# Optimization experiments

Hardware: AMD Instinct MI355X
Metric: run time of the kernel (lower is better)

Reference implementation:

```python
import jax, jax.numpy as jnp
import numpy as np

EPS_LN = 1e-5

def layer_norm(x, g, b):
    mu = x.mean(-1, keepdims=True)
    var = ((x - mu) ** 2).mean(-1, keepdims=True)
    return (x - mu) / jnp.sqrt(var + EPS_LN) * g + b

def spike(x):
    # MultiSpike: quantized spike activation, forward = clip(round(x), 0, 4)
    return jnp.clip(jnp.round(x), 0.0, 4.0)

def setup_inputs() -> dict:
    key = jax.random.key(0)
    ks = jax.random.split(key, 8)
    B, C, H, W = 16, 256, 56, 56
    hid = 128
    inp = {}
    inp['feature_map'] = jax.random.normal(ks[0], (B, C, H, W), jnp.float32)
    inp['audio_feature'] = jax.random.normal(ks[1], (B, 1, C), jnp.float32)
    # MINE params
    inp['w1'] = jax.random.normal(ks[2], (hid, 2 * C), jnp.float32) / np.sqrt(2 * C)
    inp['b1'] = jnp.zeros((hid,), jnp.float32)
    inp['g1'] = jnp.ones((hid,), jnp.float32)
    inp['beta1'] = jnp.zeros((hid,), jnp.float32)
    inp['w2'] = jax.random.normal(ks[3], (hid // 2, hid), jnp.float32) / np.sqrt(hid)
    inp['b2'] = jnp.zeros((hid // 2,), jnp.float32)
    inp['g2'] = jnp.ones((hid // 2,), jnp.float32)
    inp['beta2'] = jnp.zeros((hid // 2,), jnp.float32)
    inp['w3'] = jax.random.normal(ks[4], (1, hid // 2), jnp.float32) / np.sqrt(hid // 2)
    inp['b3'] = jnp.zeros((1,), jnp.float32)
    # MI params
    inp['pw'] = jax.random.normal(ks[5], (C, C), jnp.float32) / np.sqrt(C)
    inp['pb'] = jnp.zeros((C,), jnp.float32)
    inp['pg'] = jnp.ones((C,), jnp.float32)
    inp['pbeta'] = jnp.zeros((C,), jnp.float32)
    return inp

def reference(feature_map, audio_feature, w1, b1, g1, beta1, w2, b2, g2, beta2,
              w3, b3, pw, pb, pg, pbeta):
    B, C, H, W = feature_map.shape
    # visual tokens: [B*H*W, C]
    visual = feature_map.transpose(0, 2, 3, 1).reshape(B * H * W, C)
    # broadcast audio to every spatial position: [B*H*W, C]
    audio = jnp.broadcast_to(audio_feature[:, 0][:, None, None, :], (B, H, W, C)).reshape(B * H * W, C)
    # MINE MLP on joint features
    joint = jnp.concatenate([visual, audio], axis=1)            # [BHW, 2C]
    h = spike(layer_norm(joint @ w1.T + b1, g1, beta1))          # [BHW, 128]
    h = spike(layer_norm(h @ w2.T + b2, g2, beta2))              # [BHW, 64]
    mi = (h @ w3.T + b3)[:, 0]                                   # [BHW]
    mi_map = mi.reshape(B, 1, H * W)
    fm_flat = feature_map.reshape(B, C, H * W)
    # MI-weighted pooling: [B,1,C]
    x = jnp.einsum('bos,bcs->boc', mi_map, fm_flat)
    x = x @ pw.T + pb                                            # proj (dropout = eval identity)
    x = spike(layer_norm(x, pg, pbeta))                          # [B,1,C]
    fusion_map = jnp.einsum('bchw,bc->bchw', feature_map, x[:, 0])
    mi4 = mi_map.reshape(B, 1, H, W)
    mi4 = (mi4 - mi4.min()) / (mi4.max() - mi4.min() + 1e-6)     # global min-max norm
    return fusion_map, mi4
```

## Files before the change

### kernel.cpp

```cpp
#include <hip/hip_runtime.h>

#define HW 3136
#define NPOS 12845056

__device__ __forceinline__ unsigned fkey(float f) {
  unsigned u = __float_as_uint(f);
  return (u & 0x80000000u) ? ~u : (u | 0x80000000u);
}
__device__ __forceinline__ float funkey(unsigned u) {
  return __uint_as_float((u & 0x80000000u) ? (u & 0x7FFFFFFFu) : ~u);
}
__device__ __forceinline__ float spikef(float x) {
  return fminf(fmaxf(rintf(x), 0.0f), 4.0f);
}

__global__ __launch_bounds__(256) void prep_kernel(
    const float* __restrict__ audio, const float* __restrict__ w1,
    const float* __restrict__ b1, const float* __restrict__ w2,
    float* __restrict__ a_pre, float* __restrict__ w1t,
    float* __restrict__ w2t, float* __restrict__ pool,
    unsigned* __restrict__ mm)
{
  __shared__ float au[256];
  const int bx = blockIdx.x, t = threadIdx.x;
  if (bx < 128) {
    int idx = bx * 256 + t;
    int c = idx >> 7, j = idx & 127;
    w1t[idx] = w1[j * 512 + c];
  } else if (bx < 160) {
    int idx = (bx - 128) * 256 + t;
    int k = idx >> 6, j2 = idx & 63;
    w2t[idx] = w2[j2 * 128 + k];
  } else if (bx < 176) {
    int b = bx - 160;
    au[t] = audio[b * 256 + t];
    __syncthreads();
    int w = t >> 6, l = t & 63;
    float a0 = au[l], a1 = au[l + 64], a2 = au[l + 128], a3 = au[l + 192];
    for (int jj = 0; jj < 32; ++jj) {
      int j = w * 32 + jj;
      const float* row = w1 + j * 512 + 256;
      float s = row[l] * a0 + row[l + 64] * a1 + row[l + 128] * a2 + row[l + 192] * a3;
      #pragma unroll
      for (int off = 32; off; off >>= 1) s += __shfl_xor(s, off);
      if (l == 0) a_pre[b * 128 + j] = s + b1[j];
    }
  } else {
    for (int i = t; i < 4096; i += 256) pool[i] = 0.0f;
    if (t == 0) { mm[0] = 0xFFFFFFFFu; mm[1] = 0u; }
  }
}

__global__ __launch_bounds__(256, 3) void mlp_kernel(
    const float* __restrict__ fm, const float* __restrict__ w1t,
    const float* __restrict__ w2t, const float* __restrict__ b2,
    const float* __restrict__ w3, const float* __restrict__ b3,
    const float* __restrict__ g1, const float* __restrict__ be1,
    const float* __restrict__ g2, const float* __restrict__ be2,
    const float* __restrict__ a_pre, float* __restrict__ mi_out,
    float* __restrict__ pool, unsigned* __restrict__ mm)
{
  __shared__ float h1f[128 * 64];
  __shared__ float red[8][64];

  const int b  = blockIdx.y;
  const int s0 = blockIdx.x * 64;
  const int t  = threadIdx.x;
  const int l  = t & 63;
  const int wv = __builtin_amdgcn_readfirstlane(t >> 6);

  const float* fmblk = fm + (size_t)b * 256 * HW + s0;

  float acc[32];
  #pragma unroll
  for (int j = 0; j < 32; ++j) acc[j] = 0.f;
  {
    const float*  fp = fmblk + l;
    const float4* wr = (const float4*)(w1t + wv * 32);
    #pragma unroll 4
    for (int k = 0; k < 256; ++k) {
      float x = *fp; fp += HW;
      #pragma unroll
      for (int q = 0; q < 8; ++q) {
        float4 w4 = wr[q];
        acc[4*q+0] = fmaf(x, w4.x, acc[4*q+0]);
        acc[4*q+1] = fmaf(x, w4.y, acc[4*q+1]);
        acc[4*q+2] = fmaf(x, w4.z, acc[4*q+2]);
        acc[4*q+3] = fmaf(x, w4.w, acc[4*q+3]);
      }
      wr += 32;
    }
  }
  {
    const float4* ap = (const float4*)(a_pre + b * 128 + wv * 32);
    #pragma unroll
    for (int q = 0; q < 8; ++q) {
      float4 a4 = ap[q];
      acc[4*q+0] += a4.x; acc[4*q+1] += a4.y;
      acc[4*q+2] += a4.z; acc[4*q+3] += a4.w;
    }
  }

  float mu, inv;
  {
    float s = 0.f;
    #pragma unroll
    for (int j = 0; j < 32; ++j) s += acc[j];
    red[wv][l] = s;
    __syncthreads();
    mu = (red[0][l] + red[1][l] + red[2][l] + red[3][l]) * (1.0f/128.0f);
    float s2 = 0.f;
    #pragma unroll
    for (int j = 0; j < 32; ++j) { float d = acc[j] - mu; s2 = fmaf(d, d, s2); }
    red[4 + wv][l] = s2;
    __syncthreads();
    float var = (red[4][l] + red[5][l] + red[6][l] + red[7][l]) * (1.0f/128.0f);
    inv = 1.0f / sqrtf(var + 1e-5f);
  }

  {
    const float* gp = g1  + wv * 32;
    const float* bp = be1 + wv * 32;
    #pragma unroll
    for (int j = 0; j < 32; ++j) {
      float h = spikef((acc[j] - mu) * inv * gp[j] + bp[j]);
      h1f[(wv * 32 + j) * 64 + l] = h;
    }
  }
  __syncthreads();

  float a2[16];
  #pragma unroll
  for (int j = 0; j < 16; ++j) a2[j] = 0.f;
  {
    const float*  hp = h1f + l;
    const float4* wr = (const float4*)(w2t + wv * 16);
    #pragma unroll 4
    for (int k = 0; k < 128; ++k) {
      float h = *hp; hp += 64;
      #pragma unroll
      for (int q = 0; q < 4; ++q) {
        float4 w4 = wr[q];
        a2[4*q+0] = fmaf(h, w4.x, a2[4*q+0]);
        a2[4*q+1] = fmaf(h, w4.y, a2[4*q+1]);
        a2[4*q+2] = fmaf(h, w4.z, a2[4*q+2]);
        a2[4*q+3] = fmaf(h, w4.w, a2[4*q+3]);
      }
      wr += 16;
    }
  }
  {
    const float4* bp = (const float4*)(b2 + wv * 16);
    #pragma unroll
    for (int q = 0; q < 4; ++q) {
      float4 b4 = bp[q];
      a2[4*q+0] += b4.x; a2[4*q+1] += b4.y;
      a2[4*q+2] += b4.z; a2[4*q+3] += b4.w;
    }
  }

  float mu2, inv2;
  {
    float s = 0.f;
    #pragma unroll
    for (int j = 0; j < 16; ++j) s += a2[j];
    red[wv][l] = s;
    __syncthreads();
    mu2 = (red[0][l] + red[1][l] + red[2][l] + red[3][l]) * (1.0f/64.0f);
    float s2 = 0.f;
    #pragma unroll
    for (int j = 0; j < 16; ++j) { float d = a2[j] - mu2; s2 = fmaf(d, d, s2); }
    red[4 + wv][l] = s2;
    __syncthreads();
    float var = (red[4][l] + red[5][l] + red[6][l] + red[7][l]) * (1.0f/64.0f);
    inv2 = 1.0f / sqrtf(var + 1e-5f);
  }

  {
    const float* gp = g2  + wv * 16;
    const float* bp = be2 + wv * 16;
    const float* wp = w3  + wv * 16;
    float p = 0.f;
    #pragma unroll
    for (int j = 0; j < 16; ++j) {
      float sp = spikef((a2[j] - mu2) * inv2 * gp[j] + bp[j]);
      p = fmaf(sp, wp[j], p);
    }
    red[wv][l] = p;
  }
  __syncthreads();
  const float mi = red[0][l] + red[1][l] + red[2][l] + red[3][l] + b3[0];

  if (wv == 0) {
    mi_out[b * HW + s0 + l] = mi;
    float mn = mi, mx = mi;
    #pragma unroll
    for (int off = 32; off; off >>= 1) {
      mn = fminf(mn, __shfl_xor(mn, off));
      mx = fmaxf(mx, __shfl_xor(mx, off));
    }
    if (l == 0) {
      unsigned kmn = fkey(mn), kmx = fkey(mx);
      volatile unsigned* vmm = (volatile unsigned*)mm;
      if (kmn < vmm[0]) atomicMin(&mm[0], kmn);
      if (kmx > vmm[1]) atomicMax(&mm[1], kmx);
    }
  }

  {
    const float* fp = fmblk + l + (size_t)(wv << 6) * HW;
    #pragma unroll 4
    for (int ci = 0; ci < 64; ++ci) {
      float v = *fp * mi; fp += HW;
      #pragma unroll
      for (int off = 32; off; off >>= 1) v += __shfl_xor(v, off);
      if (l == 0) atomicAdd(&pool[b * 256 + (wv << 6) + ci], v);
    }
  }
}

__global__ __launch_bounds__(256) void scale_kernel(
    const float* __restrict__ pool, const float* __restrict__ pw,
    const float* __restrict__ pb, const float* __restrict__ pg,
    const float* __restrict__ pbeta, float* __restrict__ scale,
    const unsigned* __restrict__ mm, float* __restrict__ gpar)
{
  __shared__ float pl[256];
  __shared__ float xsh[256];
  __shared__ float rs[4], rs2[4];
  int b = blockIdx.x, t = threadIdx.x;
  pl[t] = pool[b*256 + t];
  __syncthreads();
  int w = t >> 6, l = t & 63;
  float p0 = pl[l], p1 = pl[l+64], p2 = pl[l+128], p3 = pl[l+192];
  for (int jj = 0; jj < 64; ++jj) {
    int j = w*64 + jj;
    const float* row = pw + j*256;
    float s = row[l]*p0 + row[l+64]*p1 + row[l+128]*p2 + row[l+192]*p3;
    #pragma unroll
    for (int off = 32; off; off >>= 1) s += __shfl_xor(s, off);
    if (l == 0) xsh[j] = s;
  }
  __syncthreads();
  float x = xsh[t] + pb[t];
  float s = x;
  #pragma unroll
  for (int off = 32; off; off >>= 1) s += __shfl_xor(s, off);
  if (l == 0) rs[w] = s;
  __syncthreads();
  float mu = (rs[0]+rs[1]+rs[2]+rs[3]) * (1.0f/256.0f);
  float d = x - mu;
  float s2 = d*d;
  #pragma unroll
  for (int off = 32; off; off >>= 1) s2 += __shfl_xor(s2, off);
  if (l == 0) rs2[w] = s2;
  __syncthreads();
  float var = (rs2[0]+rs2[1]+rs2[2]+rs2[3]) * (1.0f/256.0f);
  float v = d / sqrtf(var + 1e-5f) * pg[t] + pbeta[t];
  scale[b*256 + t] = spikef(v);
  if (b == 0 && t == 0) {
    float mn = funkey(mm[0]), mx = funkey(mm[1]);
    gpar[0] = mn;
    gpar[1] = mx - mn + 1e-6f;
  }
}

__global__ __launch_bounds__(256) void fuse_kernel(
    const float4* __restrict__ fm4, const float* __restrict__ scale,
    const float4* __restrict__ mi4, const float* __restrict__ gpar,
    float4* __restrict__ out4, float4* __restrict__ mi4out)
{
  const int c = blockIdx.x, b = blockIdx.y, t = threadIdx.x;
  if (c < 256) {
    float s = scale[b * 256 + c];
    size_t base = ((size_t)b * 256 + c) * 784;
    #pragma unroll
    for (int i = 0; i < 3; ++i) {
      int idx = t + i * 256;
      float4 v = fm4[base + idx];
      out4[base + idx] = make_float4(v.x*s, v.y*s, v.z*s, v.w*s);
    }
    int idx = t + 768;
    if (idx < 784) {
      float4 v = fm4[base + idx];
      out4[base + idx] = make_float4(v.x*s, v.y*s, v.z*s, v.w*s);
    }
  } else {
    float gmin = gpar[0], den = gpar[1];
    size_t base = (size_t)b * 784;
    #pragma unroll
    for (int i = 0; i < 3; ++i) {
      int idx = t + i * 256;
      float4 v = mi4[base + idx];
      mi4out[base + idx] = make_float4((v.x-gmin)/den, (v.y-gmin)/den,
                                       (v.z-gmin)/den, (v.w-gmin)/den);
    }
    int idx = t + 768;
    if (idx < 784) {
      float4 v = mi4[base + idx];
      mi4out[base + idx] = make_float4((v.x-gmin)/den, (v.y-gmin)/den,
                                       (v.z-gmin)/den, (v.w-gmin)/den);
    }
  }
}

extern "C" void kernel_launch(void* const* d_in, const int* in_sizes, int n_in,
                              void* d_out, int out_size, void* d_ws, size_t ws_size,
                              hipStream_t stream)
{
  const float* fm    = (const float*)d_in[0];
  const float* audio = (const float*)d_in[1];
  const float* w1    = (const float*)d_in[2];
  const float* b1    = (const float*)d_in[3];
  const float* g1    = (const float*)d_in[4];
  const float* be1   = (const float*)d_in[5];
  const float* w2    = (const float*)d_in[6];
  const float* b2    = (const float*)d_in[7];
  const float* g2    = (const float*)d_in[8];
  const float* be2   = (const float*)d_in[9];
  const float* w3    = (const float*)d_in[10];
  const float* b3    = (const float*)d_in[11];
  const float* pw    = (const float*)d_in[12];
  const float* pb    = (const float*)d_in[13];
  const float* pg    = (const float*)d_in[14];
  const float* pbeta = (const float*)d_in[15];

  float* ws    = (float*)d_ws;
  float* a_pre = ws;
  float* pool  = ws + 2048;
  float* scale = ws + 6144;
  float* mi    = ws + 10240;
  float* w1t   = ws + 60416;
  float* w2t   = ws + 93184;
  unsigned* mm = (unsigned*)(ws + 101376);
  float* gpar  = ws + 101378;

  float* out    = (float*)d_out;
  float* mi4out = out + NPOS;

  prep_kernel<<<177, 256, 0, stream>>>(audio, w1, b1, w2, a_pre, w1t, w2t,
                                       pool, mm);
  mlp_kernel<<<dim3(49, 16), 256, 0, stream>>>(fm, w1t, w2t, b2, w3, b3,
                                               g1, be1, g2, be2,
                                               a_pre, mi, pool, mm);
  scale_kernel<<<16, 256, 0, stream>>>(pool, pw, pb, pg, pbeta, scale, mm, gpar);
  fuse_kernel<<<dim3(257, 16), 256, 0, stream>>>((const float4*)fm, scale,
                                                 (const float4*)mi, gpar,
                                                 (float4*)out, (float4*)mi4out);
}
```

Baseline: 287.0 us.

## Split MLP work across 8 wavefronts with per-wave contiguous weight layout

Doubles mlp_kernel's block from 256 to 512 threads so each wavefront computes 16 hidden units in layer 1 and 8 in layer 2 instead of 32 and 16. This halves per-thread accumulators and raises the occupancy target. Weights are rearranged in prep_kernel so each wave reads a contiguous per-k chunk. The cost is that each fm column is loaded by 8 waves instead of 4 in the first GEMM, and the LayerNorm reductions now sum over 8 partials.

```diff
diff --git a/kernel.cpp b/kernel.cpp
--- a/kernel.cpp
+++ b/kernel.cpp
@@ -17,20 +17,22 @@
 __global__ __launch_bounds__(256) void prep_kernel(
     const float* __restrict__ audio, const float* __restrict__ w1,
     const float* __restrict__ b1, const float* __restrict__ w2,
-    float* __restrict__ a_pre, float* __restrict__ w1t,
-    float* __restrict__ w2t, float* __restrict__ pool,
+    float* __restrict__ a_pre, float* __restrict__ w1s,
+    float* __restrict__ w2s, float* __restrict__ pool,
     unsigned* __restrict__ mm)
 {
   __shared__ float au[256];
   const int bx = blockIdx.x, t = threadIdx.x;
   if (bx < 128) {
     int idx = bx * 256 + t;
-    int c = idx >> 7, j = idx & 127;
-    w1t[idx] = w1[j * 512 + c];
+    int wv = idx >> 12, k = (idx >> 4) & 255, jj = idx & 15;
+    int j = wv * 16 + jj;
+    w1s[idx] = w1[j * 512 + k];
   } else if (bx < 160) {
     int idx = (bx - 128) * 256 + t;
-    int k = idx >> 6, j2 = idx & 63;
-    w2t[idx] = w2[j2 * 128 + k];
+    int wv = idx >> 10, k = (idx >> 3) & 127, jj = idx & 7;
+    int j2 = wv * 8 + jj;
+    w2s[idx] = w2[j2 * 128 + k];
   } else if (bx < 176) {
     int b = bx - 160;
     au[t] = audio[b * 256 + t];
@@ -51,9 +53,9 @@
   }
 }
 
-__global__ __launch_bounds__(256, 3) void mlp_kernel(
-    const float* __restrict__ fm, const float* __restrict__ w1t,
-    const float* __restrict__ w2t, const float* __restrict__ b2,
+__global__ __launch_bounds__(512, 6) void mlp_kernel(
+    const float* __restrict__ fm, const float* __restrict__ w1s,
+    const float* __restrict__ w2s, const float* __restrict__ b2,
     const float* __restrict__ w3, const float* __restrict__ b3,
     const float* __restrict__ g1, const float* __restrict__ be1,
     const float* __restrict__ g2, const float* __restrict__ be2,
@@ -61,7 +63,7 @@
     float* __restrict__ pool, unsigned* __restrict__ mm)
 {
   __shared__ float h1f[128 * 64];
-  __shared__ float red[8][64];
+  __shared__ float red[16][64];
 
   const int b  = blockIdx.y;
   const int s0 = blockIdx.x * 64;
@@ -71,30 +73,39 @@
 
   const float* fmblk = fm + (size_t)b * 256 * HW + s0;
 
-  float acc[32];
-  #pragma unroll
-  for (int j = 0; j < 32; ++j) acc[j] = 0.f;
+  float acc[16];
+  #pragma unroll
+  for (int j = 0; j < 16; ++j) acc[j] = 0.f;
   {
     const float*  fp = fmblk + l;
-    const float4* wr = (const float4*)(w1t + wv * 32);
-    #pragma unroll 4
+    const float4* wr = (const float4*)(w1s + (wv << 12));
+    #pragma unroll 8
     for (int k = 0; k < 256; ++k) {
-      float x = *fp; fp += HW;
-      #pragma unroll
-      for (int q = 0; q < 8; ++q) {
-        float4 w4 = wr[q];
-        acc[4*q+0] = fmaf(x, w4.x, acc[4*q+0]);
-        acc[4*q+1] = fmaf(x, w4.y, acc[4*q+1]);
-        acc[4*q+2] = fmaf(x, w4.z, acc[4*q+2]);
-        acc[4*q+3] = fmaf(x, w4.w, acc[4*q+3]);
-      }
-      wr += 32;
-    }
-  }
-  {
-    const float4* ap = (const float4*)(a_pre + b * 128 + wv * 32);
-    #pragma unroll
-    for (int q = 0; q < 8; ++q) {
+      float x = fp[(size_t)k * HW];
+      float4 w0 = wr[4*k+0], w1v = wr[4*k+1];
+      float4 w2v = wr[4*k+2], w3v = wr[4*k+3];
+      acc[ 0] = fmaf(x, w0.x,  acc[ 0]);
+      acc[ 1] = fmaf(x, w0.y,  acc[ 1]);
+      acc[ 2] = fmaf(x, w0.z,  acc[ 2]);
+      acc[ 3] = fmaf(x, w0.w,  acc[ 3]);
+      acc[ 4] = fmaf(x, w1v.x, acc[ 4]);
+      acc[ 5] = fmaf(x, w1v.y, acc[ 5]);
+      acc[ 6] = fmaf(x, w1v.z, acc[ 6]);
+      acc[ 7] = fmaf(x, w1v.w, acc[ 7]);
+      acc[ 8] = fmaf(x, w2v.x, acc[ 8]);
+      acc[ 9] = fmaf(x, w2v.y, acc[ 9]);
+      acc[10] = fmaf(x, w2v.z, acc[10]);
+      acc[11] = fmaf(x, w2v.w, acc[11]);
+      acc[12] = fmaf(x, w3v.x, acc[12]);
+      acc[13] = fmaf(x, w3v.y, acc[13]);
+      acc[14] = fmaf(x, w3v.z, acc[14]);
+      acc[15] = fmaf(x, w3v.w, acc[15]);
+    }
+  }
+  {
+    const float4* ap = (const float4*)(a_pre + b * 128 + (wv << 4));
+    #pragma unroll
+    for (int q = 0; q < 4; ++q) {
       float4 a4 = ap[q];
       acc[4*q+0] += a4.x; acc[4*q+1] += a4.y;
       acc[4*q+2] += a4.z; acc[4*q+3] += a4.w;
@@ -105,91 +116,100 @@
   {
     float s = 0.f;
     #pragma unroll
-    for (int j = 0; j < 32; ++j) s += acc[j];
+    for (int j = 0; j < 16; ++j) s += acc[j];
     red[wv][l] = s;
     __syncthreads();
-    mu = (red[0][l] + red[1][l] + red[2][l] + red[3][l]) * (1.0f/128.0f);
+    s = 0.f;
+    #pragma unroll
+    for (int q = 0; q < 8; ++q) s += red[q][l];
+    mu = s * (1.0f/128.0f);
     float s2 = 0.f;
     #pragma unroll
-    for (int j = 0; j < 32; ++j) { float d = acc[j] - mu; s2 = fmaf(d, d, s2); }
-    red[4 + wv][l] = s2;
-    __syncthreads();
-    float var = (red[4][l] + red[5][l] + red[6][l] + red[7][l]) * (1.0f/128.0f);
-    inv = 1.0f / sqrtf(var + 1e-5f);
-  }
-
-  {
-    const float* gp = g1  + wv * 32;
-    const float* bp = be1 + wv * 32;
-    #pragma unroll
-    for (int j = 0; j < 32; ++j) {
+    for (int j = 0; j < 16; ++j) { float d = acc[j] - mu; s2 = fmaf(d, d, s2); }
+    red[8 + wv][l] = s2;
+    __syncthreads();
+    s2 = 0.f;
+    #pragma unroll
+    for (int q = 0; q < 8; ++q) s2 += red[8 + q][l];
+    inv = 1.0f / sqrtf(s2 * (1.0f/128.0f) + 1e-5f);
+  }
+
+  {
+    const float* gp = g1  + (wv << 4);
+    const float* bp = be1 + (wv << 4);
+    #pragma unroll
+    for (int j = 0; j < 16; ++j) {
       float h = spikef((acc[j] - mu) * inv * gp[j] + bp[j]);
-      h1f[(wv * 32 + j) * 64 + l] = h;
-    }
-  }
-  __syncthreads();
-
-  float a2[16];
-  #pragma unroll
-  for (int j = 0; j < 16; ++j) a2[j] = 0.f;
+      h1f[((wv << 4) + j) * 64 + l] = h;
+    }
+  }
+  __syncthreads();
+
+  float a2[8];
+  #pragma unroll
+  for (int j = 0; j < 8; ++j) a2[j] = 0.f;
   {
     const float*  hp = h1f + l;
-    const float4* wr = (const float4*)(w2t + wv * 16);
-    #pragma unroll 4
+    const float4* wr = (const float4*)(w2s + (wv << 10));
+    #pragma unroll 8
     for (int k = 0; k < 128; ++k) {
-      float h = *hp; hp += 64;
-      #pragma unroll
-      for (int q = 0; q < 4; ++q) {
-        float4 w4 = wr[q];
-        a2[4*q+0] = fmaf(h, w4.x, a2[4*q+0]);
-        a2[4*q+1] = fmaf(h, w4.y, a2[4*q+1]);
-        a2[4*q+2] = fmaf(h, w4.z, a2[4*q+2]);
-        a2[4*q+3] = fmaf(h, w4.w, a2[4*q+3]);
-      }
-      wr += 16;
-    }
-  }
-  {
-    const float4* bp = (const float4*)(b2 + wv * 16);
-    #pragma unroll
-    for (int q = 0; q < 4; ++q) {
-      float4 b4 = bp[q];
-      a2[4*q+0] += b4.x; a2[4*q+1] += b4.y;
-      a2[4*q+2] += b4.z; a2[4*q+3] += b4.w;
-    }
+      float h = hp[k * 64];
+      float4 w0 = wr[2*k+0], w1v = wr[2*k+1];
+      a2[0] = fmaf(h, w0.x,  a2[0]);
+      a2[1] = fmaf(h, w0.y,  a2[1]);
+      a2[2] = fmaf(h, w0.z,  a2[2]);
+      a2[3] = fmaf(h, w0.w,  a2[3]);
+      a2[4] = fmaf(h, w1v.x, a2[4]);
+      a2[5] = fmaf(h, w1v.y, a2[5]);
+      a2[6] = fmaf(h, w1v.z, a2[6]);
+      a2[7] = fmaf(h, w1v.w, a2[7]);
+    }
+  }
+  {
+    const float4* bp = (const float4*)(b2 + (wv << 3));
+    float4 b40 = bp[0], b41 = bp[1];
+    a2[0] += b40.x; a2[1] += b40.y; a2[2] += b40.z; a2[3] += b40.w;
+    a2[4] += b41.x; a2[5] += b41.y; a2[6] += b41.z; a2[7] += b41.w;
   }
 
   float mu2, inv2;
   {
     float s = 0.f;
     #pragma unroll
-    for (int j = 0; j < 16; ++j) s += a2[j];
+    for (int j = 0; j < 8; ++j) s += a2[j];
     red[wv][l] = s;
     __syncthreads();
-    mu2 = (red[0][l] + red[1][l] + red[2][l] + red[3][l]) * (1.0f/64.0f);
+    s = 0.f;
+    #pragma unroll
+    for (int q = 0; q < 8; ++q) s += red[q][l];
+    mu2 = s * (1.0f/64.0f);
     float s2 = 0.f;
     #pragma unroll
-    for (int j = 0; j < 16; ++j) { float d = a2[j] - mu2; s2 = fmaf(d, d, s2); }
-    red[4 + wv][l] = s2;
-    __syncthreads();
-    float var = (red[4][l] + red[5][l] + red[6][l] + red[7][l]) * (1.0f/64.0f);
-    inv2 = 1.0f / sqrtf(var + 1e-5f);
-  }
-
-  {
-    const float* gp = g2  + wv * 16;
-    const float* bp = be2 + wv * 16;
-    const float* wp = w3  + wv * 16;
+    for (int j = 0; j < 8; ++j) { float d = a2[j] - mu2; s2 = fmaf(d, d, s2); }
+    red[8 + wv][l] = s2;
+    __syncthreads();
+    s2 = 0.f;
+    #pragma unroll
+    for (int q = 0; q < 8; ++q) s2 += red[8 + q][l];
+    inv2 = 1.0f / sqrtf(s2 * (1.0f/64.0f) + 1e-5f);
+  }
+
+  {
+    const float* gp = g2  + (wv << 3);
+    const float* bp = be2 + (wv << 3);
+    const float* wp = w3  + (wv << 3);
     float p = 0.f;
     #pragma unroll
-    for (int j = 0; j < 16; ++j) {
+    for (int j = 0; j < 8; ++j) {
       float sp = spikef((a2[j] - mu2) * inv2 * gp[j] + bp[j]);
       p = fmaf(sp, wp[j], p);
     }
     red[wv][l] = p;
   }
   __syncthreads();
-  const float mi = red[0][l] + red[1][l] + red[2][l] + red[3][l] + b3[0];
+  float mi = b3[0];
+  #pragma unroll
+  for (int q = 0; q < 8; ++q) mi += red[q][l];
 
   if (wv == 0) {
     mi_out[b * HW + s0 + l] = mi;
@@ -208,13 +228,13 @@
   }
 
   {
-    const float* fp = fmblk + l + (size_t)(wv << 6) * HW;
+    const float* fp = fmblk + l + (size_t)(wv << 5) * HW;
     #pragma unroll 4
-    for (int ci = 0; ci < 64; ++ci) {
-      float v = *fp * mi; fp += HW;
+    for (int ci = 0; ci < 32; ++ci) {
+      float v = fp[(size_t)ci * HW] * mi;
       #pragma unroll
       for (int off = 32; off; off >>= 1) v += __shfl_xor(v, off);
-      if (l == 0) atomicAdd(&pool[b * 256 + (wv << 6) + ci], v);
+      if (l == 0) atomicAdd(&pool[b * 256 + (wv << 5) + ci], v);
     }
   }
 }
@@ -330,17 +350,17 @@
   float* pool  = ws + 2048;
   float* scale = ws + 6144;
   float* mi    = ws + 10240;
-  float* w1t   = ws + 60416;
-  float* w2t   = ws + 93184;
+  float* w1s   = ws + 60416;
+  float* w2s   = ws + 93184;
   unsigned* mm = (unsigned*)(ws + 101376);
   float* gpar  = ws + 101378;
 
   float* out    = (float*)d_out;
   float* mi4out = out + NPOS;
 
-  prep_kernel<<<177, 256, 0, stream>>>(audio, w1, b1, w2, a_pre, w1t, w2t,
+  prep_kernel<<<177, 256, 0, stream>>>(audio, w1, b1, w2, a_pre, w1s, w2s,
                                        pool, mm);
-  mlp_kernel<<<dim3(49, 16), 256, 0, stream>>>(fm, w1t, w2t, b2, w3, b3,
+  mlp_kernel<<<dim3(49, 16), 512, 0, stream>>>(fm, w1s, w2s, b2, w3, b3,
                                                g1, be1, g2, be2,
                                                a_pre, mi, pool, mm);
   scale_kernel<<<16, 256, 0, stream>>>(pool, pw, pb, pg, pbeta, scale, mm, gpar);
```

Measured after the change: 293.5 us. +2.3%, slower.

## Remap MLP kernel so lanes own hidden units and waves own positions

Applied to the files above, without the earlier changes.

The MLP kernel is reorganized so that each wave handles 8 spatial positions and each lane owns two hidden units of layer 1 and one unit of layer 2. LayerNorm reductions now use cross-lane shuffles instead of shared memory, and layer 2 broadcasts h1 values via readlane instead of staging them through a 32KB shared buffer. The block covers 32 positions, so the grid doubles to 98 blocks per batch, and the occupancy hint rises to 6. This removes most shared-memory traffic and barriers and raises occupancy, at the cost of many more shuffle and readlane operations and uncoalesced-looking float4 loads of feature-map rows per wave.

```diff
diff --git a/kernel.cpp b/kernel.cpp
--- a/kernel.cpp
+++ b/kernel.cpp
@@ -12,6 +12,9 @@
 }
 __device__ __forceinline__ float spikef(float x) {
   return fminf(fmaxf(rintf(x), 0.0f), 4.0f);
+}
+__device__ __forceinline__ float rdlane(float v, int src) {
+  return __int_as_float(__builtin_amdgcn_readlane(__float_as_int(v), src));
 }
 
 __global__ __launch_bounds__(256) void prep_kernel(
@@ -51,7 +54,7 @@
   }
 }
 
-__global__ __launch_bounds__(256, 3) void mlp_kernel(
+__global__ __launch_bounds__(256, 6) void mlp_kernel(
     const float* __restrict__ fm, const float* __restrict__ w1t,
     const float* __restrict__ w2t, const float* __restrict__ b2,
     const float* __restrict__ w3, const float* __restrict__ b3,
@@ -60,142 +63,126 @@
     const float* __restrict__ a_pre, float* __restrict__ mi_out,
     float* __restrict__ pool, unsigned* __restrict__ mm)
 {
-  __shared__ float h1f[128 * 64];
-  __shared__ float red[8][64];
+  __shared__ float miL[32];
 
   const int b  = blockIdx.y;
-  const int s0 = blockIdx.x * 64;
+  const int p0 = blockIdx.x * 32;
   const int t  = threadIdx.x;
   const int l  = t & 63;
   const int wv = __builtin_amdgcn_readfirstlane(t >> 6);
-
-  const float* fmblk = fm + (size_t)b * 256 * HW + s0;
-
-  float acc[32];
-  #pragma unroll
-  for (int j = 0; j < 32; ++j) acc[j] = 0.f;
-  {
-    const float*  fp = fmblk + l;
-    const float4* wr = (const float4*)(w1t + wv * 32);
+  const int pos0 = p0 + wv * 8;
+  const int j0 = 2 * l;
+
+  float acc0[8], acc1[8];
+  #pragma unroll
+  for (int p = 0; p < 8; ++p) { acc0[p] = 0.f; acc1[p] = 0.f; }
+  {
+    const float* xrow = fm + (size_t)b * 256 * HW + pos0;
+    const float* wrow = w1t + j0;
     #pragma unroll 4
     for (int k = 0; k < 256; ++k) {
-      float x = *fp; fp += HW;
-      #pragma unroll
-      for (int q = 0; q < 8; ++q) {
-        float4 w4 = wr[q];
-        acc[4*q+0] = fmaf(x, w4.x, acc[4*q+0]);
-        acc[4*q+1] = fmaf(x, w4.y, acc[4*q+1]);
-        acc[4*q+2] = fmaf(x, w4.z, acc[4*q+2]);
-        acc[4*q+3] = fmaf(x, w4.w, acc[4*q+3]);
+      float4 xa = *(const float4*)(xrow + (size_t)k * HW);
+      float4 xb = *(const float4*)(xrow + (size_t)k * HW + 4);
+      float2 w = *(const float2*)(wrow + k * 128);
+      acc0[0] = fmaf(xa.x, w.x, acc0[0]); acc1[0] = fmaf(xa.x, w.y, acc1[0]);
+      acc0[1] = fmaf(xa.y, w.x, acc0[1]); acc1[1] = fmaf(xa.y, w.y, acc1[1]);
+      acc0[2] = fmaf(xa.z, w.x, acc0[2]); acc1[2] = fmaf(xa.z, w.y, acc1[2]);
+      acc0[3] = fmaf(xa.w, w.x, acc0[3]); acc1[3] = fmaf(xa.w, w.y, acc1[3]);
+      acc0[4] = fmaf(xb.x, w.x, acc0[4]); acc1[4] = fmaf(xb.x, w.y, acc1[4]);
+      acc0[5] = fmaf(xb.y, w.x, acc0[5]); acc1[5] = fmaf(xb.y, w.y, acc1[5]);
+      acc0[6] = fmaf(xb.z, w.x, acc0[6]); acc1[6] = fmaf(xb.z, w.y, acc1[6]);
+      acc0[7] = fmaf(xb.w, w.x, acc0[7]); acc1[7] = fmaf(xb.w, w.y, acc1[7]);
+    }
+  }
+  {
+    float2 ap = *(const float2*)(a_pre + b * 128 + j0);
+    #pragma unroll
+    for (int p = 0; p < 8; ++p) { acc0[p] += ap.x; acc1[p] += ap.y; }
+  }
+
+  float mu_[8];
+  #pragma unroll
+  for (int p = 0; p < 8; ++p) {
+    float s = acc0[p] + acc1[p];
+    #pragma unroll
+    for (int off = 32; off; off >>= 1) s += __shfl_xor(s, off);
+    mu_[p] = s * (1.0f/128.0f);
+  }
+  float h1a[8], h1b[8];
+  {
+    float2 gv = *(const float2*)(g1 + j0);
+    float2 bv = *(const float2*)(be1 + j0);
+    #pragma unroll
+    for (int p = 0; p < 8; ++p) {
+      float d0 = acc0[p] - mu_[p], d1 = acc1[p] - mu_[p];
+      float s2 = d0 * d0 + d1 * d1;
+      #pragma unroll
+      for (int off = 32; off; off >>= 1) s2 += __shfl_xor(s2, off);
+      float inv = 1.0f / sqrtf(s2 * (1.0f/128.0f) + 1e-5f);
+      h1a[p] = spikef(d0 * inv * gv.x + bv.x);
+      h1b[p] = spikef(d1 * inv * gv.y + bv.y);
+    }
+  }
+
+  float acc2[8];
+  #pragma unroll
+  for (int p = 0; p < 8; ++p) acc2[p] = 0.f;
+  {
+    const float* w2base = w2t + l;
+    #pragma unroll 2
+    for (int kp = 0; kp < 64; ++kp) {
+      float wA = w2base[(2*kp) * 64];
+      float wB = w2base[(2*kp+1) * 64];
+      #pragma unroll
+      for (int p = 0; p < 8; ++p) {
+        float xA = rdlane(h1a[p], kp);
+        float xB = rdlane(h1b[p], kp);
+        acc2[p] = fmaf(xB, wB, fmaf(xA, wA, acc2[p]));
       }
-      wr += 32;
-    }
-  }
-  {
-    const float4* ap = (const float4*)(a_pre + b * 128 + wv * 32);
-    #pragma unroll
-    for (int q = 0; q < 8; ++q) {
-      float4 a4 = ap[q];
-      acc[4*q+0] += a4.x; acc[4*q+1] += a4.y;
-      acc[4*q+2] += a4.z; acc[4*q+3] += a4.w;
-    }
-  }
-
-  float mu, inv;
-  {
-    float s = 0.f;
-    #pragma unroll
-    for (int j = 0; j < 32; ++j) s += acc[j];
-    red[wv][l] = s;
-    __syncthreads();
-    mu = (red[0][l] + red[1][l] + red[2][l] + red[3][l]) * (1.0f/128.0f);
-    float s2 = 0.f;
-    #pragma unroll
-    for (int j = 0; j < 32; ++j) { float d = acc[j] - mu; s2 = fmaf(d, d, s2); }
-    red[4 + wv][l] = s2;
-    __syncthreads();
-    float var = (red[4][l] + red[5][l] + red[6][l] + red[7][l]) * (1.0f/128.0f);
-    inv = 1.0f / sqrtf(var + 1e-5f);
-  }
-
-  {
-    const float* gp = g1  + wv * 32;
-    const float* bp = be1 + wv * 32;
-    #pragma unroll
-    for (int j = 0; j < 32; ++j) {
-      float h = spikef((acc[j] - mu) * inv * gp[j] + bp[j]);
-      h1f[(wv * 32 + j) * 64 + l] = h;
-    }
-  }
-  __syncthreads();
-
-  float a2[16];
-  #pragma unroll
-  for (int j = 0; j < 16; ++j) a2[j] = 0.f;
-  {
-    const float*  hp = h1f + l;
-    const float4* wr = (const float4*)(w2t + wv * 16);
-    #pragma unroll 4
-    for (int k = 0; k < 128; ++k) {
-      float h = *hp; hp += 64;
-      #pragma unroll
-      for (int q = 0; q < 4; ++q) {
-        float4 w4 = wr[q];
-        a2[4*q+0] = fmaf(h, w4.x, a2[4*q+0]);
-        a2[4*q+1] = fmaf(h, w4.y, a2[4*q+1]);
-        a2[4*q+2] = fmaf(h, w4.z, a2[4*q+2]);
-        a2[4*q+3] = fmaf(h, w4.w, a2[4*q+3]);
-      }
-      wr += 16;
-    }
-  }
-  {
-    const float4* bp = (const float4*)(b2 + wv * 16);
-    #pragma unroll
-    for (int q = 0; q < 4; ++q) {
-      float4 b4 = bp[q];
-      a2[4*q+0] += b4.x; a2[4*q+1] += b4.y;
-      a2[4*q+2] += b4.z; a2[4*q+3] += b4.w;
-    }
-  }
-
-  float mu2, inv2;
-  {
-    float s = 0.f;
-    #pragma unroll
-    for (int j = 0; j < 16; ++j) s += a2[j];
-    red[wv][l] = s;
-    __syncthreads();
-    mu2 = (red[0][l] + red[1][l] + red[2][l] + red[3][l]) * (1.0f/64.0f);
-    float s2 = 0.f;
-    #pragma unroll
-    for (int j = 0; j < 16; ++j) { float d = a2[j] - mu2; s2 = fmaf(d, d, s2); }
-    red[4 + wv][l] = s2;
-    __syncthreads();
-    float var = (red[4][l] + red[5][l] + red[6][l] + red[7][l]) * (1.0f/64.0f);
-    inv2 = 1.0f / sqrtf(var + 1e-5f);
-  }
-
-  {
-    const float* gp = g2  + wv * 16;
-    const float* bp = be2 + wv * 16;
-    const float* wp = w3  + wv * 16;
-    float p = 0.f;
-    #pragma unroll
-    for (int j = 0; j < 16; ++j) {
-      float sp = spikef((a2[j] - mu2) * inv2 * gp[j] + bp[j]);
-      p = fmaf(sp, wp[j], p);
-    }
-    red[wv][l] = p;
-  }
-  __syncthreads();
-  const float mi = red[0][l] + red[1][l] + red[2][l] + red[3][l] + b3[0];
+    }
+  }
+
+  const float b2l = b2[l];
+  #pragma unroll
+  for (int p = 0; p < 8; ++p) acc2[p] += b2l;
+  float miv[8];
+  {
+    const float g2l = g2[l], be2l = be2[l], w3l = w3[l];
+    const float b3v = b3[0];
+    #pragma unroll
+    for (int p = 0; p < 8; ++p) {
+      float s = acc2[p];
+      #pragma unroll
+      for (int off = 32; off; off >>= 1) s += __shfl_xor(s, off);
+      float mu2 = s * (1.0f/64.0f);
+      float d = acc2[p] - mu2;
+      float s2 = d * d;
+      #pragma unroll
+      for (int off = 32; off; off >>= 1) s2 += __shfl_xor(s2, off);
+      float inv2 = 1.0f / sqrtf(s2 * (1.0f/64.0f) + 1e-5f);
+      float sp = spikef(d * inv2 * g2l + be2l) * w3l;
+      #pragma unroll
+      for (int off = 32; off; off >>= 1) sp += __shfl_xor(sp, off);
+      miv[p] = sp + b3v;
+    }
+  }
+
+  {
+    float m = 0.f;
+    #pragma unroll
+    for (int p = 0; p < 8; ++p) m = (l == p) ? miv[p] : m;
+    if (l < 8) {
+      mi_out[b * HW + pos0 + l] = m;
+      miL[wv * 8 + l] = m;
+    }
+  }
+  __syncthreads();
 
   if (wv == 0) {
-    mi_out[b * HW + s0 + l] = mi;
-    float mn = mi, mx = mi;
-    #pragma unroll
-    for (int off = 32; off; off >>= 1) {
+    float v = miL[l & 31];
+    float mn = v, mx = v;
+    #pragma unroll
+    for (int off = 16; off; off >>= 1) {
       mn = fminf(mn, __shfl_xor(mn, off));
       mx = fmaxf(mx, __shfl_xor(mx, off));
     }
@@ -208,13 +195,15 @@
   }
 
   {
-    const float* fp = fmblk + l + (size_t)(wv << 6) * HW;
+    const int pos = l & 31, ph = l >> 5;
+    const float mval = miL[pos];
+    const float* fp = fm + ((size_t)(b * 256 + wv * 64 + ph * 32)) * HW + p0 + pos;
     #pragma unroll 4
-    for (int ci = 0; ci < 64; ++ci) {
-      float v = *fp * mi; fp += HW;
-      #pragma unroll
-      for (int off = 32; off; off >>= 1) v += __shfl_xor(v, off);
-      if (l == 0) atomicAdd(&pool[b * 256 + (wv << 6) + ci], v);
+    for (int ci = 0; ci < 32; ++ci) {
+      float v = fp[(size_t)ci * HW] * mval;
+      #pragma unroll
+      for (int off = 16; off; off >>= 1) v += __shfl_xor(v, off);
+      if (pos == 0) atomicAdd(&pool[b * 256 + wv * 64 + ph * 32 + ci], v);
     }
   }
 }
@@ -340,7 +329,7 @@
 
   prep_kernel<<<177, 256, 0, stream>>>(audio, w1, b1, w2, a_pre, w1t, w2t,
                                        pool, mm);
-  mlp_kernel<<<dim3(49, 16), 256, 0, stream>>>(fm, w1t, w2t, b2, w3, b3,
+  mlp_kernel<<<dim3(98, 16), 256, 0, stream>>>(fm, w1t, w2t, b2, w3, b3,
                                                g1, be1, g2, be2,
                                                a_pre, mi, pool, mm);
   scale_kernel<<<16, 256, 0, stream>>>(pool, pw, pb, pg, pbeta, scale, mm, gpar);
```

Result: slower. 325.3 us (+13.3%).

## Stage W1 chunks in LDS via async loads and remap layer-2 MLP to lanes

Applied to the files above, without the earlier changes.

Layer 1 now copies W1 into shared memory in four 64-row chunks with global_load_lds and reads weights from LDS instead of issuing uniform global float4 loads per k. Layer 2 is remapped so each lane owns one output neuron and each wave handles 16 positions, so LayerNorm-2 and the w3 dot product become wave shuffles rather than cross-wave shared-memory reductions with barriers. The aim is to cut global and scalar-cache weight traffic and remove barriers. The cost is extra syncs per chunk and many more shuffle reductions (three per position, sixteen positions per wave).

```diff
diff --git a/kernel.cpp b/kernel.cpp
--- a/kernel.cpp
+++ b/kernel.cpp
@@ -60,8 +60,9 @@
     const float* __restrict__ a_pre, float* __restrict__ mi_out,
     float* __restrict__ pool, unsigned* __restrict__ mm)
 {
-  __shared__ float h1f[128 * 64];
-  __shared__ float red[8][64];
+  __shared__ __align__(16) float wbuf[8192];
+  __shared__ float red[2][4][64];
+  __shared__ float miL[64];
 
   const int b  = blockIdx.y;
   const int s0 = blockIdx.x * 64;
@@ -70,25 +71,54 @@
   const int wv = __builtin_amdgcn_readfirstlane(t >> 6);
 
   const float* fmblk = fm + (size_t)b * 256 * HW + s0;
+  const float* fp = fmblk + l;
 
   float acc[32];
   #pragma unroll
   for (int j = 0; j < 32; ++j) acc[j] = 0.f;
-  {
-    const float*  fp = fmblk + l;
-    const float4* wr = (const float4*)(w1t + wv * 32);
-    #pragma unroll 4
-    for (int k = 0; k < 256; ++k) {
-      float x = *fp; fp += HW;
-      #pragma unroll
-      for (int q = 0; q < 8; ++q) {
-        float4 w4 = wr[q];
-        acc[4*q+0] = fmaf(x, w4.x, acc[4*q+0]);
-        acc[4*q+1] = fmaf(x, w4.y, acc[4*q+1]);
-        acc[4*q+2] = fmaf(x, w4.z, acc[4*q+2]);
-        acc[4*q+3] = fmaf(x, w4.w, acc[4*q+3]);
-      }
-      wr += 32;
+
+  #pragma unroll 1
+  for (int ch = 0; ch < 4; ++ch) {
+    if (ch) __syncthreads();
+    {
+      const float* src = w1t + ch * 8192 + wv * 256 + l * 4;
+      float* dst = wbuf + wv * 256;
+      #pragma unroll
+      for (int i = 0; i < 8; ++i)
+        __builtin_amdgcn_global_load_lds(
+            (const __attribute__((address_space(1))) void*)(src + i * 1024),
+            (__attribute__((address_space(3))) void*)(dst + i * 1024), 16, 0, 0);
+    }
+    __syncthreads();
+    const float* wrow = wbuf + wv * 32;
+    #pragma unroll 2
+    for (int k = 0; k < 64; ++k) {
+      float x = fp[(size_t)(ch * 64 + k) * HW];
+      const float* wk = wrow + k * 128;
+      float4 q0 = *(const float4*)(wk);
+      float4 q1 = *(const float4*)(wk + 4);
+      float4 q2 = *(const float4*)(wk + 8);
+      float4 q3 = *(const float4*)(wk + 12);
+      float4 q4 = *(const float4*)(wk + 16);
+      float4 q5 = *(const float4*)(wk + 20);
+      float4 q6 = *(const float4*)(wk + 24);
+      float4 q7 = *(const float4*)(wk + 28);
+      acc[ 0] = fmaf(x, q0.x, acc[ 0]); acc[ 1] = fmaf(x, q0.y, acc[ 1]);
+      acc[ 2] = fmaf(x, q0.z, acc[ 2]); acc[ 3] = fmaf(x, q0.w, acc[ 3]);
+      acc[ 4] = fmaf(x, q1.x, acc[ 4]); acc[ 5] = fmaf(x, q1.y, acc[ 5]);
+      acc[ 6] = fmaf(x, q1.z, acc[ 6]); acc[ 7] = fmaf(x, q1.w, acc[ 7]);
+      acc[ 8] = fmaf(x, q2.x, acc[ 8]); acc[ 9] = fmaf(x, q2.y, acc[ 9]);
+      acc[10] = fmaf(x, q2.z, acc[10]); acc[11] = fmaf(x, q2.w, acc[11]);
+      acc[12] = fmaf(x, q3.x, acc[12]); acc[13] = fmaf(x, q3.y, acc[13]);
+      acc[14] = fmaf(x, q3.z, acc[14]); acc[15] = fmaf(x, q3.w, acc[15]);
+      acc[16] = fmaf(x, q4.x, acc[16]); acc[17] = fmaf(x, q4.y, acc[17]);
+      acc[18] = fmaf(x, q4.z, acc[18]); acc[19] = fmaf(x, q4.w, acc[19]);
+      acc[20] = fmaf(x, q5.x, acc[20]); acc[21] = fmaf(x, q5.y, acc[21]);
+      acc[22] = fmaf(x, q5.z, acc[22]); acc[23] = fmaf(x, q5.w, acc[23]);
+      acc[24] = fmaf(x, q6.x, acc[24]); acc[25] = fmaf(x, q6.y, acc[25]);
+      acc[26] = fmaf(x, q6.z, acc[26]); acc[27] = fmaf(x, q6.w, acc[27]);
+      acc[28] = fmaf(x, q7.x, acc[28]); acc[29] = fmaf(x, q7.y, acc[29]);
+      acc[30] = fmaf(x, q7.z, acc[30]); acc[31] = fmaf(x, q7.w, acc[31]);
     }
   }
   {
@@ -106,15 +136,15 @@
     float s = 0.f;
     #pragma unroll
     for (int j = 0; j < 32; ++j) s += acc[j];
-    red[wv][l] = s;
+    red[0][wv][l] = s;
     __syncthreads();
-    mu = (red[0][l] + red[1][l] + red[2][l] + red[3][l]) * (1.0f/128.0f);
+    mu = (red[0][0][l] + red[0][1][l] + red[0][2][l] + red[0][3][l]) * (1.0f/128.0f);
     float s2 = 0.f;
     #pragma unroll
     for (int j = 0; j < 32; ++j) { float d = acc[j] - mu; s2 = fmaf(d, d, s2); }
-    red[4 + wv][l] = s2;
+    red[1][wv][l] = s2;
     __syncthreads();
-    float var = (red[4][l] + red[5][l] + red[6][l] + red[7][l]) * (1.0f/128.0f);
+    float var = (red[1][0][l] + red[1][1][l] + red[1][2][l] + red[1][3][l]) * (1.0f/128.0f);
     inv = 1.0f / sqrtf(var + 1e-5f);
   }
 
@@ -124,76 +154,77 @@
     #pragma unroll
     for (int j = 0; j < 32; ++j) {
       float h = spikef((acc[j] - mu) * inv * gp[j] + bp[j]);
-      h1f[(wv * 32 + j) * 64 + l] = h;
+      wbuf[(wv * 32 + j) * 64 + l] = h;
     }
   }
   __syncthreads();
 
   float a2[16];
   #pragma unroll
-  for (int j = 0; j < 16; ++j) a2[j] = 0.f;
-  {
-    const float*  hp = h1f + l;
-    const float4* wr = (const float4*)(w2t + wv * 16);
-    #pragma unroll 4
-    for (int k = 0; k < 128; ++k) {
-      float h = *hp; hp += 64;
-      #pragma unroll
-      for (int q = 0; q < 4; ++q) {
-        float4 w4 = wr[q];
-        a2[4*q+0] = fmaf(h, w4.x, a2[4*q+0]);
-        a2[4*q+1] = fmaf(h, w4.y, a2[4*q+1]);
-        a2[4*q+2] = fmaf(h, w4.z, a2[4*q+2]);
-        a2[4*q+3] = fmaf(h, w4.w, a2[4*q+3]);
-      }
-      wr += 16;
-    }
-  }
-  {
-    const float4* bp = (const float4*)(b2 + wv * 16);
-    #pragma unroll
-    for (int q = 0; q < 4; ++q) {
-      float4 b4 = bp[q];
-      a2[4*q+0] += b4.x; a2[4*q+1] += b4.y;
-      a2[4*q+2] += b4.z; a2[4*q+3] += b4.w;
-    }
-  }
-
-  float mu2, inv2;
-  {
-    float s = 0.f;
-    #pragma unroll
-    for (int j = 0; j < 16; ++j) s += a2[j];
-    red[wv][l] = s;
-    __syncthreads();
-    mu2 = (red[0][l] + red[1][l] + red[2][l] + red[3][l]) * (1.0f/64.0f);
-    float s2 = 0.f;
-    #pragma unroll
-    for (int j = 0; j < 16; ++j) { float d = a2[j] - mu2; s2 = fmaf(d, d, s2); }
-    red[4 + wv][l] = s2;
-    __syncthreads();
-    float var = (red[4][l] + red[5][l] + red[6][l] + red[7][l]) * (1.0f/64.0f);
-    inv2 = 1.0f / sqrtf(var + 1e-5f);
-  }
-
-  {
-    const float* gp = g2  + wv * 16;
-    const float* bp = be2 + wv * 16;
-    const float* wp = w3  + wv * 16;
-    float p = 0.f;
-    #pragma unroll
-    for (int j = 0; j < 16; ++j) {
-      float sp = spikef((a2[j] - mu2) * inv2 * gp[j] + bp[j]);
-      p = fmaf(sp, wp[j], p);
-    }
-    red[wv][l] = p;
-  }
-  __syncthreads();
-  const float mi = red[0][l] + red[1][l] + red[2][l] + red[3][l] + b3[0];
+  for (int p = 0; p < 16; ++p) a2[p] = 0.f;
+  {
+    const float* hrow = wbuf + wv * 16;
+    const float* w2p  = w2t + l;
+    #pragma unroll 2
+    for (int k2 = 0; k2 < 128; ++k2) {
+      float w = w2p[k2 * 64];
+      const float* hk = hrow + k2 * 64;
+      float4 x0 = *(const float4*)(hk);
+      float4 x1 = *(const float4*)(hk + 4);
+      float4 x2 = *(const float4*)(hk + 8);
+      float4 x3 = *(const float4*)(hk + 12);
+      a2[ 0] = fmaf(x0.x, w, a2[ 0]); a2[ 1] = fmaf(x0.y, w, a2[ 1]);
+      a2[ 2] = fmaf(x0.z, w, a2[ 2]); a2[ 3] = fmaf(x0.w, w, a2[ 3]);
+      a2[ 4] = fmaf(x1.x, w, a2[ 4]); a2[ 5] = fmaf(x1.y, w, a2[ 5]);
+      a2[ 6] = fmaf(x1.z, w, a2[ 6]); a2[ 7] = fmaf(x1.w, w, a2[ 7]);
+      a2[ 8] = fmaf(x2.x, w, a2[ 8]); a2[ 9] = fmaf(x2.y, w, a2[ 9]);
+      a2[10] = fmaf(x2.z, w, a2[10]); a2[11] = fmaf(x2.w, w, a2[11]);
+      a2[12] = fmaf(x3.x, w, a2[12]); a2[13] = fmaf(x3.y, w, a2[13]);
+      a2[14] = fmaf(x3.z, w, a2[14]); a2[15] = fmaf(x3.w, w, a2[15]);
+    }
+  }
+  {
+    const float b2l = b2[l];
+    #pragma unroll
+    for (int p = 0; p < 16; ++p) a2[p] += b2l;
+  }
+
+  float miv[16];
+  {
+    const float g2l = g2[l], be2l = be2[l], w3l = w3[l];
+    const float b3v = b3[0];
+    #pragma unroll
+    for (int p = 0; p < 16; ++p) {
+      float s = a2[p];
+      #pragma unroll
+      for (int off = 32; off; off >>= 1) s += __shfl_xor(s, off);
+      float mu2 = s * (1.0f/64.0f);
+      float d = a2[p] - mu2;
+      float s2 = d * d;
+      #pragma unroll
+      for (int off = 32; off; off >>= 1) s2 += __shfl_xor(s2, off);
+      float inv2 = 1.0f / sqrtf(s2 * (1.0f/64.0f) + 1e-5f);
+      float sp = spikef(d * inv2 * g2l + be2l) * w3l;
+      #pragma unroll
+      for (int off = 32; off; off >>= 1) sp += __shfl_xor(sp, off);
+      miv[p] = sp + b3v;
+    }
+  }
+
+  {
+    float m = miv[0];
+    #pragma unroll
+    for (int p = 1; p < 16; ++p) m = (l == p) ? miv[p] : m;
+    if (l < 16) {
+      mi_out[b * HW + s0 + wv * 16 + l] = m;
+      miL[wv * 16 + l] = m;
+    }
+  }
+  __syncthreads();
 
   if (wv == 0) {
-    mi_out[b * HW + s0 + l] = mi;
-    float mn = mi, mx = mi;
+    float v = miL[l];
+    float mn = v, mx = v;
     #pragma unroll
     for (int off = 32; off; off >>= 1) {
       mn = fminf(mn, __shfl_xor(mn, off));
@@ -208,10 +239,11 @@
   }
 
   {
-    const float* fp = fmblk + l + (size_t)(wv << 6) * HW;
+    const float mval = miL[l];
+    const float* fp2 = fmblk + l + (size_t)(wv << 6) * HW;
     #pragma unroll 4
     for (int ci = 0; ci < 64; ++ci) {
-      float v = *fp * mi; fp += HW;
+      float v = fp2[(size_t)ci * HW] * mval;
       #pragma unroll
       for (int off = 32; off; off >>= 1) v += __shfl_xor(v, off);
       if (l == 0) atomicAdd(&pool[b * 256 + (wv << 6) + ci], v);
```

Result: slower. 327.5 us (+14.1%).
